# Kernel tuning notes

Measured on AMD Instinct MI355X. Metric: run time of the kernel, lower is better.

## Reference

```python
import jax, jax.numpy as jnp
import numpy as np

B, N, C, H = 8, 2048, 512, 8
D = C // H  # head_dim = 64

def rope(t):
    # t: (B, H, T, D); rotate even/odd interleaved pairs
    T = t.shape[2]
    inv_freq = 1.0 / (10000.0 ** (jnp.arange(0, D, 2, dtype=t.dtype) / D))  # (D/2,)
    pos = jnp.arange(T, dtype=t.dtype)
    freqs = pos[:, None] * inv_freq[None, :]            # (T, D/2)
    cos, sin = jnp.cos(freqs), jnp.sin(freqs)           # broadcast over (B,H)
    t_un = t[..., 0::2]
    t_ev = t[..., 1::2]
    r_un = t_un * cos - t_ev * sin
    r_ev = t_un * sin + t_ev * cos
    # interleave back: (..., D/2, 2) -> (..., D)
    return jnp.stack([r_un, r_ev], axis=-1).reshape(t.shape)

def setup_inputs() -> dict:
    key = jax.random.key(0)
    k1, k2, k3, k4 = jax.random.split(key, 4)
    x = jax.random.normal(k1, (B, N, C), dtype=jnp.float32)
    mask = jax.random.normal(k2, (B, N), dtype=jnp.float32)
    W_qkv = jax.random.normal(k3, (3 * C, C), dtype=jnp.float32) * (1.0 / np.sqrt(C))
    W_proj = jax.random.normal(k4, (C, C), dtype=jnp.float32) * (1.0 / np.sqrt(C))
    b_proj = jnp.zeros((C,), dtype=jnp.float32)
    return {"x": x, "mask": mask, "W_qkv": W_qkv, "W_proj": W_proj,
            "b_proj": b_proj, "num_cls_token": 1}

def reference(x, mask, W_qkv, W_proj, b_proj, num_cls_token):
    scale = D ** (-0.5)
    qkv = jnp.einsum('bnc,fc->bnf', x, W_qkv)             # (B,N,3C)
    qkv = qkv.reshape(B, N, 3, H, D).transpose(2, 0, 3, 1, 4)  # (3,B,H,N,D)
    q, k, v = qkv[0], qkv[1], qkv[2]
    nc = num_cls_token
    if nc > 0:
        q = jnp.concatenate([q[:, :, :nc], rope(q[:, :, nc:])], axis=2)
        k = jnp.concatenate([k[:, :, :nc], rope(k[:, :, nc:])], axis=2)
    else:
        q, k = rope(q), rope(k)
    attn = jnp.einsum('bhnd,bhmd->bhnm', q * scale, k)    # (B,H,N,N)
    attn = attn + mask[:, None, None, :] + mask[:, None, :, None]
    attn = jax.nn.softmax(attn, axis=-1)
    out = jnp.einsum('bhnm,bhmd->bhnd', attn, v)          # (B,H,N,D)
    out = out.transpose(0, 2, 1, 3).reshape(B, N, C)
    return out @ W_proj.T + b_proj
```

## Files before the change

### kernel.cpp

```cpp
#include <hip/hip_runtime.h>
#include <cmath>

#define BB 8
#define NN 2048
#define CC 512
#define HH 8
#define DD 64
#define FF 1536
#define MM (BB*NN)

typedef _Float16 half_t;
typedef __attribute__((ext_vector_type(8))) _Float16 half8;
typedef __attribute__((ext_vector_type(4))) _Float16 half4;
typedef __attribute__((ext_vector_type(4))) float floatx4;

#define LOG2E 1.44269504088896f

typedef const __attribute__((address_space(1))) unsigned int* gas_ptr;
typedef __attribute__((address_space(3))) unsigned int* las_ptr;
__device__ __forceinline__ void gld16(const half_t* g, half_t* l) {
  __builtin_amdgcn_global_load_lds((gas_ptr)g, (las_ptr)l, 16, 0, 0);
}

__global__ __launch_bounds__(256) void cvt_kernel(
    const float* __restrict__ s, half_t* __restrict__ d, int n8) {
  int i = blockIdx.x * 256 + threadIdx.x;
  if (i < n8) {
    float4 a = ((const float4*)s)[i * 2], b = ((const float4*)s)[i * 2 + 1];
    half8 h;
    h[0] = (half_t)a.x; h[1] = (half_t)a.y; h[2] = (half_t)a.z; h[3] = (half_t)a.w;
    h[4] = (half_t)b.x; h[5] = (half_t)b.y; h[6] = (half_t)b.z; h[7] = (half_t)b.w;
    ((half8*)d)[i] = h;
  }
}

__global__ __launch_bounds__(256) void qkv_mfma_kernel(
    const half_t* __restrict__ Ah,
    const half_t* __restrict__ Bh,
    const int*   __restrict__ ncp,
    half_t* __restrict__ Qh, half_t* __restrict__ Kh, half_t* __restrict__ Vt)
{
  __shared__ union {
    struct { half_t A[128 * 32]; half_t B[128 * 32]; } s;
    half_t T[4][64 * 68];
  } sm;

  const int tid  = threadIdx.x;
  const int wave = tid >> 6, lane = tid & 63;
  const int L15  = lane & 15, quad = lane >> 4;
  const int wm = (wave & 1) * 64, wn = (wave >> 1) * 64;
  const int m0 = blockIdx.x * 128;
  const int f0 = blockIdx.y * 128;

  const int srow = lane >> 2;
  const int scolh = (lane & 3) * 8;
  const half_t* Ag = Ah + (size_t)(m0 + wave * 16 + srow) * CC + scolh;
  const half_t* Bg = Bh + (size_t)(f0 + wave * 16 + srow) * CC + scolh;
  half_t* Al = &sm.s.A[(wave * 16) * 32];
  half_t* Bl = &sm.s.B[(wave * 16) * 32];

  floatx4 acc[4][4];
#pragma unroll
  for (int i = 0; i < 4; ++i)
#pragma unroll
    for (int j = 0; j < 4; ++j) acc[i][j] = (floatx4){0.f, 0.f, 0.f, 0.f};

  for (int k0 = 0; k0 < CC; k0 += 32) {
    __syncthreads();
    gld16(Ag + k0,            Al);
    gld16(Ag + k0 + 64 * CC,  Al + 64 * 32);
    gld16(Bg + k0,            Bl);
    gld16(Bg + k0 + 64 * CC,  Bl + 64 * 32);
    __syncthreads();
    half8 af[4], bf[4];
#pragma unroll
    for (int mi = 0; mi < 4; ++mi)
      af[mi] = *(const half8*)&sm.s.A[(wm + mi * 16 + L15) * 32 + quad * 8];
#pragma unroll
    for (int ni = 0; ni < 4; ++ni)
      bf[ni] = *(const half8*)&sm.s.B[(wn + ni * 16 + L15) * 32 + quad * 8];
#pragma unroll
    for (int mi = 0; mi < 4; ++mi)
#pragma unroll
      for (int ni = 0; ni < 4; ++ni)
        acc[mi][ni] = __builtin_amdgcn_mfma_f32_16x16x32_f16(af[mi], bf[ni], acc[mi][ni], 0, 0, 0);
  }

  const int which = f0 >> 9;
  const int b     = m0 >> 11;
  const int n_base = (m0 & 2047) + wm;

  if (which < 2) {
    const int nc = *ncp;
    half_t* dst = which ? Kh : Qh;
    const float qscale = which ? 1.0f : (0.125f * LOG2E);
#pragma unroll
    for (int ni = 0; ni < 4; ++ni) {
      const int f = f0 + wn + ni * 16 + L15;
      const int h = (f >> 6) & 7;
      const int d = f & 63;
      const float invf = __powf(10000.0f, -(float)(d & ~1) * (1.0f / 64.0f));
      const float sgn = (d & 1) ? 1.0f : -1.0f;
#pragma unroll
      for (int mi = 0; mi < 4; ++mi)
#pragma unroll
        for (int r = 0; r < 4; ++r) {
          const int n = n_base + mi * 16 + quad * 4 + r;
          float v = acc[mi][ni][r];
          float p = __shfl_xor(v, 1, 64);
          if (n >= nc) {
            float sv, cv;
            __sincosf((float)(n - nc) * invf, &sv, &cv);
            v = v * cv + sgn * p * sv;
          }
          dst[(((size_t)(b * HH + h) * NN + n) << 6) + d] = (half_t)(v * qscale);
        }
    }
  } else {
    __syncthreads();
#pragma unroll
    for (int ni = 0; ni < 4; ++ni)
#pragma unroll
      for (int mi = 0; mi < 4; ++mi)
#pragma unroll
        for (int r = 0; r < 4; ++r)
          sm.T[wave][(ni * 16 + L15) * 68 + mi * 16 + quad * 4 + r] = (half_t)acc[mi][ni][r];
    __syncthreads();
    const int h = ((f0 + wn) >> 6) & 7;
    const size_t gbase = ((size_t)(b * HH + h) * DD + lane) * NN + n_base;
#pragma unroll
    for (int c = 0; c < 8; ++c)
      *(half8*)(Vt + gbase + c * 8) = *(const half8*)&sm.T[wave][lane * 68 + c * 8];
  }
}

#define KPAD 72
#define PPAD 68
#define EXP2_OFF 4.3280851f
__global__ __launch_bounds__(256, 4) void flash_mfma_kernel(
    const half_t* __restrict__ Qh,
    const half_t* __restrict__ Kh,
    const half_t* __restrict__ Vt,
    const float*  __restrict__ mask,
    half_t* __restrict__ O)
{
  __shared__ half_t Ks[64 * KPAD];
  __shared__ half_t Vs[64 * KPAD];
  __shared__ half_t Ps[4][32 * PPAD];

  const int tid  = threadIdx.x;
  const int wave = tid >> 6;
  const int lane = tid & 63;
  const int L15  = lane & 15;
  const int quad = lane >> 4;

  const int bid  = blockIdx.x;
  const int xcd  = bid & 7;
  const int slot = bid >> 3;
  const int qt   = slot & 15;
  const int head = (slot >> 4) * 8 + xcd;
  const int b    = head >> 3;
  const int h    = head & 7;

  const half_t* Kt_base = Kh + ((((size_t)b * HH + h) * NN) << 6);
  const half_t* Vt_base = Vt + ((((size_t)b * HH + h) * DD) * NN);

  half8 qa[2][2];
#pragma unroll
  for (int g = 0; g < 2; ++g) {
    const half_t* Qrow =
        Qh + ((((size_t)b * HH + h) * NN + qt * 128 + wave * 32 + g * 16 + L15) << 6);
    qa[g][0] = *(const half8*)(Qrow + quad * 8);
    qa[g][1] = *(const half8*)(Qrow + 32 + quad * 8);
  }

  floatx4 oacc[2][4];
#pragma unroll
  for (int g = 0; g < 2; ++g)
#pragma unroll
    for (int sd = 0; sd < 4; ++sd) oacc[g][sd] = (floatx4){0.f, 0.f, 0.f, 0.f};
  float l_part[2][4] = {};

  const int sn = tid >> 3;
  const int sp = (tid & 7) * 8;
  half8 kreg[2], vreg[2];
  float mk_cur[4], mk_nxt[4];
#define LOAD_KV(kt)                                                               \
  {                                                                               \
    kreg[0] = *(const half8*)(Kt_base + (((size_t)(kt) * 64 + sn) << 6) + sp);    \
    kreg[1] = *(const half8*)(Kt_base + (((size_t)(kt) * 64 + sn + 32) << 6) + sp); \
    vreg[0] = *(const half8*)(Vt_base + (size_t)sn * NN + (kt) * 64 + sp);        \
    vreg[1] = *(const half8*)(Vt_base + (size_t)(sn + 32) * NN + (kt) * 64 + sp); \
  }
#define LOAD_MK(kt, dstm)                                                         \
  {                                                                               \
    _Pragma("unroll")                                                             \
    for (int s = 0; s < 4; ++s)                                                   \
      dstm[s] = mask[(size_t)b * NN + (kt) * 64 + s * 16 + L15] * LOG2E - EXP2_OFF; \
  }

  LOAD_KV(0)
  LOAD_MK(0, mk_cur)

  for (int kt = 0; kt < NN / 64; ++kt) {
    __syncthreads();
    *(half8*)&Ks[sn * KPAD + sp]        = kreg[0];
    *(half8*)&Ks[(sn + 32) * KPAD + sp] = kreg[1];
    *(half8*)&Vs[sn * KPAD + sp]        = vreg[0];
    *(half8*)&Vs[(sn + 32) * KPAD + sp] = vreg[1];
    __syncthreads();
    if (kt + 1 < NN / 64) {
      LOAD_KV(kt + 1)
      LOAD_MK(kt + 1, mk_nxt)
    }

    floatx4 S[2][4];
#pragma unroll
    for (int s = 0; s < 4; ++s) {
      half8 kb0 = *(const half8*)&Ks[(s * 16 + L15) * KPAD + quad * 8];
      half8 kb1 = *(const half8*)&Ks[(s * 16 + L15) * KPAD + 32 + quad * 8];
#pragma unroll
      for (int g = 0; g < 2; ++g) {
        floatx4 a = (floatx4){0.f, 0.f, 0.f, 0.f};
        a = __builtin_amdgcn_mfma_f32_16x16x32_f16(qa[g][0], kb0, a, 0, 0, 0);
        a = __builtin_amdgcn_mfma_f32_16x16x32_f16(qa[g][1], kb1, a, 0, 0, 0);
        S[g][s] = a;
      }
    }

#pragma unroll
    for (int g = 0; g < 2; ++g)
#pragma unroll
      for (int s = 0; s < 4; ++s)
#pragma unroll
        for (int r = 0; r < 4; ++r) {
          float p = __builtin_amdgcn_exp2f(S[g][s][r] + mk_cur[s]);
          l_part[g][r] += p;
          Ps[wave][(g * 16 + quad * 4 + r) * PPAD + s * 16 + L15] = (half_t)p;
        }

    half8 pa[2][2];
#pragma unroll
    for (int g = 0; g < 2; ++g) {
      pa[g][0] = *(const half8*)&Ps[wave][(g * 16 + L15) * PPAD + quad * 8];
      pa[g][1] = *(const half8*)&Ps[wave][(g * 16 + L15) * PPAD + 32 + quad * 8];
    }

#pragma unroll
    for (int sd = 0; sd < 4; ++sd) {
      half8 vb0 = *(const half8*)&Vs[(sd * 16 + L15) * KPAD + quad * 8];
      half8 vb1 = *(const half8*)&Vs[(sd * 16 + L15) * KPAD + 32 + quad * 8];
#pragma unroll
      for (int g = 0; g < 2; ++g) {
        oacc[g][sd] = __builtin_amdgcn_mfma_f32_16x16x32_f16(pa[g][0], vb0, oacc[g][sd], 0, 0, 0);
        oacc[g][sd] = __builtin_amdgcn_mfma_f32_16x16x32_f16(pa[g][1], vb1, oacc[g][sd], 0, 0, 0);
      }
    }

#pragma unroll
    for (int s = 0; s < 4; ++s) mk_cur[s] = mk_nxt[s];
  }

#pragma unroll
  for (int g = 0; g < 2; ++g)
#pragma unroll
    for (int r = 0; r < 4; ++r) {
#pragma unroll
      for (int off = 1; off < 16; off <<= 1)
        l_part[g][r] += __shfl_xor(l_part[g][r], off, 64);
    }

#pragma unroll
  for (int g = 0; g < 2; ++g)
#pragma unroll
    for (int r = 0; r < 4; ++r) {
      const float invl = 1.0f / l_part[g][r];
      const int row = qt * 128 + wave * 32 + g * 16 + quad * 4 + r;
#pragma unroll
      for (int sd = 0; sd < 4; ++sd)
        O[(((size_t)b * NN + row) << 9) + (h << 6) + sd * 16 + L15] =
            (half_t)(oacc[g][sd][r] * invl);
    }
}

__global__ __launch_bounds__(256) void proj_mfma_kernel(
    const half_t* __restrict__ Ah,
    const half_t* __restrict__ Bh,
    const float* __restrict__ bias,
    float* __restrict__ out)
{
  __shared__ half_t As[128 * 32];
  __shared__ half_t Bs[128 * 32];

  const int tid  = threadIdx.x;
  const int wave = tid >> 6, lane = tid & 63;
  const int L15  = lane & 15, quad = lane >> 4;
  const int wm = (wave & 1) * 64, wn = (wave >> 1) * 64;
  const int m0 = blockIdx.x * 128;
  const int f0 = blockIdx.y * 128;

  const int srow = lane >> 2;
  const int scolh = (lane & 3) * 8;
  const half_t* Ag = Ah + (size_t)(m0 + wave * 16 + srow) * CC + scolh;
  const half_t* Bg = Bh + (size_t)(f0 + wave * 16 + srow) * CC + scolh;
  half_t* Al = &As[(wave * 16) * 32];
  half_t* Bl = &Bs[(wave * 16) * 32];

  floatx4 acc[4][4];
#pragma unroll
  for (int i = 0; i < 4; ++i)
#pragma unroll
    for (int j = 0; j < 4; ++j) acc[i][j] = (floatx4){0.f, 0.f, 0.f, 0.f};

  for (int k0 = 0; k0 < CC; k0 += 32) {
    __syncthreads();
    gld16(Ag + k0,           Al);
    gld16(Ag + k0 + 64 * CC, Al + 64 * 32);
    gld16(Bg + k0,           Bl);
    gld16(Bg + k0 + 64 * CC, Bl + 64 * 32);
    __syncthreads();
    half8 af[4], bf[4];
#pragma unroll
    for (int mi = 0; mi < 4; ++mi)
      af[mi] = *(const half8*)&As[(wm + mi * 16 + L15) * 32 + quad * 8];
#pragma unroll
    for (int ni = 0; ni < 4; ++ni)
      bf[ni] = *(const half8*)&Bs[(wn + ni * 16 + L15) * 32 + quad * 8];
#pragma unroll
    for (int mi = 0; mi < 4; ++mi)
#pragma unroll
      for (int ni = 0; ni < 4; ++ni)
        acc[mi][ni] = __builtin_amdgcn_mfma_f32_16x16x32_f16(af[mi], bf[ni], acc[mi][ni], 0, 0, 0);
  }

#pragma unroll
  for (int ni = 0; ni < 4; ++ni) {
    const int f = f0 + wn + ni * 16 + L15;
    const float bv = bias[f];
#pragma unroll
    for (int mi = 0; mi < 4; ++mi)
#pragma unroll
      for (int r = 0; r < 4; ++r)
        out[(size_t)(m0 + wm + mi * 16 + quad * 4 + r) * CC + f] = acc[mi][ni][r] + bv;
  }
}

extern "C" void kernel_launch(void* const* d_in, const int* in_sizes, int n_in,
                              void* d_out, int out_size, void* d_ws, size_t ws_size,
                              hipStream_t stream) {
  const float* x     = (const float*)d_in[0];
  const float* mask  = (const float*)d_in[1];
  const float* Wqkv  = (const float*)d_in[2];
  const float* Wproj = (const float*)d_in[3];
  const float* bproj = (const float*)d_in[4];
  const int*   ncp   = (const int*)d_in[5];
  float* out = (float*)d_out;

  const size_t per = (size_t)BB * HH * NN * DD;
  half_t* xh  = (half_t*)d_ws;
  half_t* Wqh = xh + (size_t)MM * CC;
  half_t* Wph = Wqh + (size_t)FF * CC;
  half_t* Qh  = Wph + (size_t)CC * CC;
  half_t* Kh  = Qh + per;
  half_t* Vt  = Kh + per;
  half_t* Oh  = Vt + per;

  cvt_kernel<<<dim3(MM * CC / 8 / 256), 256, 0, stream>>>(x, xh, MM * CC / 8);
  cvt_kernel<<<dim3(FF * CC / 8 / 256), 256, 0, stream>>>(Wqkv, Wqh, FF * CC / 8);
  cvt_kernel<<<dim3(CC * CC / 8 / 256), 256, 0, stream>>>(Wproj, Wph, CC * CC / 8);

  qkv_mfma_kernel<<<dim3(MM / 128, FF / 128), 256, 0, stream>>>(xh, Wqh, ncp, Qh, Kh, Vt);
  flash_mfma_kernel<<<dim3(BB * HH * (NN / 128)), 256, 0, stream>>>(Qh, Kh, Vt, mask, Oh);
  proj_mfma_kernel<<<dim3(MM / 128, CC / 128), 256, 0, stream>>>(Oh, Wph, bproj, out);
}
```

Baseline: 267.6 us.

## Rewrite flash attention with 32x32 MFMA, transposed S, register P and async LDS loads

The attention kernel moves from 16x16x32 MFMA tiles to 32x32x16 tiles and computes S transposed (K as the A operand), so each lane holds a column of probabilities. Those probabilities are repacked through cross-half lane shuffles instead of a per-wave shared-memory round trip. K/V tiles are now double-buffered in XOR-swizzled LDS via global_load_lds direct copies, with one barrier per iteration. The aim is to remove LDS traffic for P, bank conflicts and register staging of K/V, at the cost of more complex lane mapping and a heavier final normalization that needs a shuffle per output element.

```diff
diff --git a/kernel.cpp b/kernel.cpp
--- a/kernel.cpp
+++ b/kernel.cpp
@@ -13,6 +13,8 @@
 typedef __attribute__((ext_vector_type(8))) _Float16 half8;
 typedef __attribute__((ext_vector_type(4))) _Float16 half4;
 typedef __attribute__((ext_vector_type(4))) float floatx4;
+typedef __attribute__((ext_vector_type(16))) float floatx16;
+typedef __attribute__((ext_vector_type(4))) float fx4;
 
 #define LOG2E 1.44269504088896f
 
@@ -134,8 +136,6 @@
   }
 }
 
-#define KPAD 72
-#define PPAD 68
 #define EXP2_OFF 4.3280851f
 __global__ __launch_bounds__(256, 4) void flash_mfma_kernel(
     const half_t* __restrict__ Qh,
@@ -144,15 +144,14 @@
     const float*  __restrict__ mask,
     half_t* __restrict__ O)
 {
-  __shared__ half_t Ks[64 * KPAD];
-  __shared__ half_t Vs[64 * KPAD];
-  __shared__ half_t Ps[4][32 * PPAD];
+  __shared__ half_t KV[2][2][64 * 64];
 
   const int tid  = threadIdx.x;
   const int wave = tid >> 6;
   const int lane = tid & 63;
-  const int L15  = lane & 15;
-  const int quad = lane >> 4;
+  const int l31  = lane & 31;
+  const int hi   = lane >> 5;
+  const int l7   = lane & 7;
 
   const int bid  = blockIdx.x;
   const int xcd  = bid & 7;
@@ -163,124 +162,129 @@
   const int h    = head & 7;
 
   const half_t* Kt_base = Kh + ((((size_t)b * HH + h) * NN) << 6);
-  const half_t* Vt_base = Vt + ((((size_t)b * HH + h) * DD) * NN);
-
-  half8 qa[2][2];
-#pragma unroll
-  for (int g = 0; g < 2; ++g) {
-    const half_t* Qrow =
-        Qh + ((((size_t)b * HH + h) * NN + qt * 128 + wave * 32 + g * 16 + L15) << 6);
-    qa[g][0] = *(const half8*)(Qrow + quad * 8);
-    qa[g][1] = *(const half8*)(Qrow + 32 + quad * 8);
-  }
-
-  floatx4 oacc[2][4];
-#pragma unroll
-  for (int g = 0; g < 2; ++g)
-#pragma unroll
-    for (int sd = 0; sd < 4; ++sd) oacc[g][sd] = (floatx4){0.f, 0.f, 0.f, 0.f};
-  float l_part[2][4] = {};
-
-  const int sn = tid >> 3;
-  const int sp = (tid & 7) * 8;
-  half8 kreg[2], vreg[2];
-  float mk_cur[4], mk_nxt[4];
-#define LOAD_KV(kt)                                                               \
-  {                                                                               \
-    kreg[0] = *(const half8*)(Kt_base + (((size_t)(kt) * 64 + sn) << 6) + sp);    \
-    kreg[1] = *(const half8*)(Kt_base + (((size_t)(kt) * 64 + sn + 32) << 6) + sp); \
-    vreg[0] = *(const half8*)(Vt_base + (size_t)sn * NN + (kt) * 64 + sp);        \
-    vreg[1] = *(const half8*)(Vt_base + (size_t)(sn + 32) * NN + (kt) * 64 + sp); \
-  }
-#define LOAD_MK(kt, dstm)                                                         \
-  {                                                                               \
-    _Pragma("unroll")                                                             \
-    for (int s = 0; s < 4; ++s)                                                   \
-      dstm[s] = mask[(size_t)b * NN + (kt) * 64 + s * 16 + L15] * LOG2E - EXP2_OFF; \
-  }
-
-  LOAD_KV(0)
-  LOAD_MK(0, mk_cur)
-
+  const half_t* Vt_base = Vt + (((size_t)b * HH + h) * DD) * NN;
+
+  half8 qf[4];
+  {
+    const half_t* Qp =
+        Qh + ((((size_t)b * HH + h) * NN + qt * 128 + wave * 32 + l31) << 6) + hi * 8;
+#pragma unroll
+    for (int kd = 0; kd < 4; ++kd) qf[kd] = *(const half8*)(Qp + kd * 16);
+  }
+
+  const int r8  = lane >> 3;
+  const int dof = ((l7 ^ r8) << 3);
+  const half_t* kg0 = Kt_base + (((size_t)(wave * 16 + r8)) << 6) + dof;
+  const half_t* kg1 = kg0 + (8 << 6);
+  const half_t* vg0 = Vt_base + (size_t)(wave * 16 + r8) * NN + dof;
+  const half_t* vg1 = vg0 + (size_t)8 * NN;
+
+  int adK[4], adV[4];
+#pragma unroll
+  for (int c = 0; c < 4; ++c) {
+    const int sw = ((((c << 1) | hi) ^ l7) << 4);
+    adK[c] = l31 * 128 + sw;
+    adV[c] = 8192 + l31 * 128 + sw;
+  }
+  const char* L = (const char*)KV;
+
+  floatx16 acc[2];
+#pragma unroll
+  for (int dt = 0; dt < 2; ++dt)
+#pragma unroll
+    for (int r = 0; r < 16; ++r) acc[dt][r] = 0.f;
+  float l_part = 0.f;
+
+  const float* mkb = mask + (size_t)b * NN + hi * 4;
+
+  gld16(kg0, &KV[0][0][wave * 1024]);
+  gld16(kg1, &KV[0][0][wave * 1024 + 512]);
+  gld16(vg0, &KV[0][1][wave * 1024]);
+  gld16(vg1, &KV[0][1][wave * 1024 + 512]);
+  __syncthreads();
+
+#pragma unroll 1
   for (int kt = 0; kt < NN / 64; ++kt) {
-    __syncthreads();
-    *(half8*)&Ks[sn * KPAD + sp]        = kreg[0];
-    *(half8*)&Ks[(sn + 32) * KPAD + sp] = kreg[1];
-    *(half8*)&Vs[sn * KPAD + sp]        = vreg[0];
-    *(half8*)&Vs[(sn + 32) * KPAD + sp] = vreg[1];
-    __syncthreads();
-    if (kt + 1 < NN / 64) {
-      LOAD_KV(kt + 1)
-      LOAD_MK(kt + 1, mk_nxt)
+    if (kt != NN / 64 - 1) {
+      kg0 += 4096; kg1 += 4096; vg0 += 64; vg1 += 64;
+      const int nb = (kt & 1) ^ 1;
+      gld16(kg0, &KV[nb][0][wave * 1024]);
+      gld16(kg1, &KV[nb][0][wave * 1024 + 512]);
+      gld16(vg0, &KV[nb][1][wave * 1024]);
+      gld16(vg1, &KV[nb][1][wave * 1024 + 512]);
     }
 
-    floatx4 S[2][4];
-#pragma unroll
-    for (int s = 0; s < 4; ++s) {
-      half8 kb0 = *(const half8*)&Ks[(s * 16 + L15) * KPAD + quad * 8];
-      half8 kb1 = *(const half8*)&Ks[(s * 16 + L15) * KPAD + 32 + quad * 8];
-#pragma unroll
-      for (int g = 0; g < 2; ++g) {
-        floatx4 a = (floatx4){0.f, 0.f, 0.f, 0.f};
-        a = __builtin_amdgcn_mfma_f32_16x16x32_f16(qa[g][0], kb0, a, 0, 0, 0);
-        a = __builtin_amdgcn_mfma_f32_16x16x32_f16(qa[g][1], kb1, a, 0, 0, 0);
-        S[g][s] = a;
+#pragma unroll
+    for (int t = 0; t < 2; ++t) {
+      fx4 m4[4];
+#pragma unroll
+      for (int r2 = 0; r2 < 4; ++r2)
+        m4[r2] = *(const fx4*)(mkb + t * 32 + r2 * 8);
+
+      floatx16 S;
+#pragma unroll
+      for (int r = 0; r < 16; ++r) S[r] = 0.f;
+#pragma unroll
+      for (int kd = 0; kd < 4; ++kd) {
+        half8 kf = *(const half8*)(L + (adK[kd] + t * 4096));
+        S = __builtin_amdgcn_mfma_f32_32x32x16_f16(kf, qf[kd], S, 0, 0, 0);
+      }
+
+#pragma unroll
+      for (int r = 0; r < 16; ++r) {
+        float p = __builtin_amdgcn_exp2f(fmaf(m4[r >> 2][r & 3], LOG2E, S[r] - EXP2_OFF));
+        l_part += p;
+        S[r] = p;
+      }
+
+      unsigned W[4][2];
+#pragma unroll
+      for (int r2 = 0; r2 < 4; ++r2)
+#pragma unroll
+        for (int u = 0; u < 2; ++u) {
+          union { half_t hh[2]; unsigned w; } pk;
+          pk.hh[0] = (half_t)S[r2 * 4 + 2 * u];
+          pk.hh[1] = (half_t)S[r2 * 4 + 2 * u + 1];
+          W[r2][u] = pk.w;
+        }
+
+#pragma unroll
+      for (int ksl = 0; ksl < 2; ++ksl) {
+        unsigned A0 = W[2 * ksl][0],     A1 = W[2 * ksl][1];
+        unsigned B0 = W[2 * ksl + 1][0], B1 = W[2 * ksl + 1][1];
+        unsigned pA0 = __shfl_xor(A0, 32, 64), pA1 = __shfl_xor(A1, 32, 64);
+        unsigned pB0 = __shfl_xor(B0, 32, 64), pB1 = __shfl_xor(B1, 32, 64);
+        union { unsigned u[4]; half8 v; } pw;
+        pw.u[0] = hi ? pB0 : A0;
+        pw.u[1] = hi ? pB1 : A1;
+        pw.u[2] = hi ? B0 : pA0;
+        pw.u[3] = hi ? B1 : pA1;
+        const int ks = t * 2 + ksl;
+#pragma unroll
+        for (int dt = 0; dt < 2; ++dt) {
+          half8 vf = *(const half8*)(L + (adV[ks] + dt * 4096));
+          acc[dt] = __builtin_amdgcn_mfma_f32_32x32x16_f16(pw.v, vf, acc[dt], 0, 0, 0);
+        }
       }
     }
 
-#pragma unroll
-    for (int g = 0; g < 2; ++g)
-#pragma unroll
-      for (int s = 0; s < 4; ++s)
-#pragma unroll
-        for (int r = 0; r < 4; ++r) {
-          float p = __builtin_amdgcn_exp2f(S[g][s][r] + mk_cur[s]);
-          l_part[g][r] += p;
-          Ps[wave][(g * 16 + quad * 4 + r) * PPAD + s * 16 + L15] = (half_t)p;
-        }
-
-    half8 pa[2][2];
-#pragma unroll
-    for (int g = 0; g < 2; ++g) {
-      pa[g][0] = *(const half8*)&Ps[wave][(g * 16 + L15) * PPAD + quad * 8];
-      pa[g][1] = *(const half8*)&Ps[wave][(g * 16 + L15) * PPAD + 32 + quad * 8];
-    }
-
-#pragma unroll
-    for (int sd = 0; sd < 4; ++sd) {
-      half8 vb0 = *(const half8*)&Vs[(sd * 16 + L15) * KPAD + quad * 8];
-      half8 vb1 = *(const half8*)&Vs[(sd * 16 + L15) * KPAD + 32 + quad * 8];
-#pragma unroll
-      for (int g = 0; g < 2; ++g) {
-        oacc[g][sd] = __builtin_amdgcn_mfma_f32_16x16x32_f16(pa[g][0], vb0, oacc[g][sd], 0, 0, 0);
-        oacc[g][sd] = __builtin_amdgcn_mfma_f32_16x16x32_f16(pa[g][1], vb1, oacc[g][sd], 0, 0, 0);
-      }
-    }
-
-#pragma unroll
-    for (int s = 0; s < 4; ++s) mk_cur[s] = mk_nxt[s];
-  }
-
-#pragma unroll
-  for (int g = 0; g < 2; ++g)
-#pragma unroll
-    for (int r = 0; r < 4; ++r) {
-#pragma unroll
-      for (int off = 1; off < 16; off <<= 1)
-        l_part[g][r] += __shfl_xor(l_part[g][r], off, 64);
-    }
-
-#pragma unroll
-  for (int g = 0; g < 2; ++g)
-#pragma unroll
-    for (int r = 0; r < 4; ++r) {
-      const float invl = 1.0f / l_part[g][r];
-      const int row = qt * 128 + wave * 32 + g * 16 + quad * 4 + r;
-#pragma unroll
-      for (int sd = 0; sd < 4; ++sd)
-        O[(((size_t)b * NN + row) << 9) + (h << 6) + sd * 16 + L15] =
-            (half_t)(oacc[g][sd][r] * invl);
-    }
+    mkb += 64;
+    __syncthreads();
+#pragma unroll
+    for (int c = 0; c < 4; ++c) { adK[c] ^= 16384; adV[c] ^= 16384; }
+  }
+
+  l_part += __shfl_xor(l_part, 32, 64);
+
+  const size_t orow = (size_t)b * NN + qt * 128 + wave * 32;
+#pragma unroll
+  for (int r = 0; r < 16; ++r) {
+    const int ql  = (r & 3) + 8 * (r >> 2) + 4 * hi;
+    const float iv = 1.0f / __shfl(l_part, ql, 64);
+    const size_t ro = ((orow + ql) << 9) + (h << 6) + l31;
+    O[ro]      = (half_t)(acc[0][r] * iv);
+    O[ro + 32] = (half_t)(acc[1][r] * iv);
+  }
 }
 
 __global__ __launch_bounds__(256) void proj_mfma_kernel(
```

After: 280.7 us. 1.05x slower.
